# Kernel tuning notes

Measured on AMD Instinct MI355X. Metric: run time of the kernel, lower is better.

The kernel has to match this reference:

```python
import jax, jax.numpy as jnp
import numpy as np

R_ITERS = 3
EPSILON = 1e-7


def squash(s, epsilon=EPSILON, axis=-1):
    # s: (..., dim); v = |s|^2/(1+|s|^2) * s/(|s|+eps)
    s_norm = jnp.linalg.norm(s, axis=axis, keepdims=True)
    sq = jnp.square(s_norm)
    return sq / (1.0 + sq) * (s / (s_norm + epsilon))


def setup_inputs() -> dict:
    key = jax.random.key(0)
    k1, k2 = jax.random.split(key)
    B, P, Dp = 128, 1152, 8     # batch, n_primary_caps, dim_primary_caps
    S, Ds = 32, 16              # n_secondary_caps, dim_secondary_caps
    x = jax.random.normal(k1, (B, P, Dp), dtype=jnp.float32)
    W = jax.random.normal(k2, (S, P, Ds, Dp), dtype=jnp.float32) * 0.05
    return {"x": x, "W": W}


def reference(x, W):
    # u_hat[b,s,p,j] = sum_i W[s,p,j,i] * x[b,p,i]  (replaces tf.map_fn+matmul)
    u_hat = jnp.einsum('spji,bpi->bspj', W, x)  # (B, S, P, Ds)
    B, S, P, Ds = u_hat.shape
    b_logits = jnp.zeros((B, S, P), dtype=u_hat.dtype)
    v = None
    for _ in range(R_ITERS):
        c = jax.nn.softmax(b_logits, axis=-1)                # (B, S, P)
        s_vec = jnp.einsum('bsp,bspj->bsj', c, u_hat)        # (B, S, Ds)
        v = squash(s_vec)                                    # (B, S, Ds)
        agreement = jnp.einsum('bsj,bspj->bsp', v, u_hat)    # (B, S, P)
        b_logits = b_logits + agreement
    return v  # (B, n_secondary_caps, dim_secondary_caps)
```

## Files before the change

kernel.cpp:

```cpp
#include <hip/hip_runtime.h>

#define P_SZ 1152
#define DP 8
#define DS 16
#define NTHR 512
#define NQ 128
#define PT 9
#define NW 8

__global__ __launch_bounds__(NTHR, 4)
void caps_routing5(const float* __restrict__ x, const float* __restrict__ W,
                   float* __restrict__ out) {
    __shared__ float red[2][NW][2][17];

    const int t    = threadIdx.x;
    const int lane = t & 63;
    const int jq   = t & 3;
    const int pq   = t >> 2;
    const int w    = t >> 6;
    const int bid  = blockIdx.x;
    const int s    = bid & 31;
    const int b0   = (bid >> 5) << 1;

    float uh0[PT][4], uh1[PT][4];

    const float* xb0 = x + (size_t)b0 * (P_SZ * DP);
    const float* xb1 = xb0 + P_SZ * DP;

    #pragma unroll
    for (int r = 0; r < PT; ++r) {
        const int p = r * NQ + pq;
        const float* wp = W + (size_t)(s * P_SZ + p) * (DS * DP) + jq * DP;
        const float4 xa0 = *(const float4*)(xb0 + p * DP);
        const float4 xa1 = *(const float4*)(xb0 + p * DP + 4);
        const float4 xc0 = *(const float4*)(xb1 + p * DP);
        const float4 xc1 = *(const float4*)(xb1 + p * DP + 4);
        #pragma unroll
        for (int jj = 0; jj < 4; ++jj) {
            const float4 w0 = *(const float4*)(wp + jj * 32);
            const float4 w1 = *(const float4*)(wp + jj * 32 + 4);
            uh0[r][jj] = w0.x*xa0.x + w0.y*xa0.y + w0.z*xa0.z + w0.w*xa0.w
                       + w1.x*xa1.x + w1.y*xa1.y + w1.z*xa1.z + w1.w*xa1.w;
            uh1[r][jj] = w0.x*xc0.x + w0.y*xc0.y + w0.z*xc0.z + w0.w*xc0.w
                       + w1.x*xc1.x + w1.y*xc1.y + w1.z*xc1.z + w1.w*xc1.w;
        }
    }

    float sv0[4], sv1[4];
    #pragma unroll
    for (int jj = 0; jj < 4; ++jj) {
        float a = 0.f, c = 0.f;
        #pragma unroll
        for (int r = 0; r < PT; ++r) { a += uh0[r][jj]; c += uh1[r][jj]; }
        sv0[jj] = a; sv1[jj] = c;
    }
    #pragma unroll
    for (int off = 4; off < 64; off <<= 1) {
        #pragma unroll
        for (int jj = 0; jj < 4; ++jj) {
            sv0[jj] += __shfl_xor(sv0[jj], off);
            sv1[jj] += __shfl_xor(sv1[jj], off);
        }
    }
    if (lane < 4) {
        #pragma unroll
        for (int jj = 0; jj < 4; ++jj) {
            red[0][w][0][jq + 4*jj] = sv0[jj];
            red[0][w][1][jq + 4*jj] = sv1[jj];
        }
    }
    __syncthreads();
    #pragma unroll
    for (int jj = 0; jj < 4; ++jj) { sv0[jj] = 0.f; sv1[jj] = 0.f; }
    #pragma unroll
    for (int ww = 0; ww < NW; ++ww) {
        #pragma unroll
        for (int jj = 0; jj < 4; ++jj) {
            sv0[jj] += red[0][ww][0][jq + 4*jj];
            sv1[jj] += red[0][ww][1][jq + 4*jj];
        }
    }
    #pragma unroll
    for (int jj = 0; jj < 4; ++jj) { sv0[jj] *= (1.f / P_SZ); sv1[jj] *= (1.f / P_SZ); }

    float sq0 = sv0[0]*sv0[0] + sv0[1]*sv0[1] + sv0[2]*sv0[2] + sv0[3]*sv0[3];
    float sq1 = sv1[0]*sv1[0] + sv1[1]*sv1[1] + sv1[2]*sv1[2] + sv1[3]*sv1[3];
    sq0 += __shfl_xor(sq0, 1); sq0 += __shfl_xor(sq0, 2);
    sq1 += __shfl_xor(sq1, 1); sq1 += __shfl_xor(sq1, 2);
    float f0 = sq0 / (1.f + sq0) / (sqrtf(sq0) + 1e-7f);
    float f1 = sq1 / (1.f + sq1) / (sqrtf(sq1) + 1e-7f);
    float va0[4], va1[4];
    #pragma unroll
    for (int jj = 0; jj < 4; ++jj) { va0[jj] = f0 * sv0[jj]; va1[jj] = f1 * sv1[jj]; }

    #pragma unroll
    for (int it = 1; it < 3; ++it) {
        float es0 = 0.f, es1 = 0.f;
        #pragma unroll
        for (int jj = 0; jj < 4; ++jj) { sv0[jj] = 0.f; sv1[jj] = 0.f; }
        #pragma unroll
        for (int r = 0; r < PT; ++r) {
            float d0 = va0[0]*uh0[r][0] + va0[1]*uh0[r][1]
                     + va0[2]*uh0[r][2] + va0[3]*uh0[r][3];
            float d1 = va1[0]*uh1[r][0] + va1[1]*uh1[r][1]
                     + va1[2]*uh1[r][2] + va1[3]*uh1[r][3];
            d0 += __shfl_xor(d0, 1); d0 += __shfl_xor(d0, 2);
            d1 += __shfl_xor(d1, 1); d1 += __shfl_xor(d1, 2);
            const float e0 = __expf(d0);
            const float e1 = __expf(d1);
            es0 += e0; es1 += e1;
            #pragma unroll
            for (int jj = 0; jj < 4; ++jj) {
                sv0[jj] += e0 * uh0[r][jj];
                sv1[jj] += e1 * uh1[r][jj];
            }
        }
        #pragma unroll
        for (int off = 4; off < 64; off <<= 1) {
            es0 += __shfl_xor(es0, off);
            es1 += __shfl_xor(es1, off);
            #pragma unroll
            for (int jj = 0; jj < 4; ++jj) {
                sv0[jj] += __shfl_xor(sv0[jj], off);
                sv1[jj] += __shfl_xor(sv1[jj], off);
            }
        }
        const int buf = it & 1;
        if (lane < 4) {
            #pragma unroll
            for (int jj = 0; jj < 4; ++jj) {
                red[buf][w][0][jq + 4*jj] = sv0[jj];
                red[buf][w][1][jq + 4*jj] = sv1[jj];
            }
            if (lane == 0) { red[buf][w][0][16] = es0; red[buf][w][1][16] = es1; }
        }
        __syncthreads();
        es0 = 0.f; es1 = 0.f;
        #pragma unroll
        for (int jj = 0; jj < 4; ++jj) { sv0[jj] = 0.f; sv1[jj] = 0.f; }
        #pragma unroll
        for (int ww = 0; ww < NW; ++ww) {
            es0 += red[buf][ww][0][16];
            es1 += red[buf][ww][1][16];
            #pragma unroll
            for (int jj = 0; jj < 4; ++jj) {
                sv0[jj] += red[buf][ww][0][jq + 4*jj];
                sv1[jj] += red[buf][ww][1][jq + 4*jj];
            }
        }
        const float r0 = 1.f / es0, r1 = 1.f / es1;
        #pragma unroll
        for (int jj = 0; jj < 4; ++jj) { sv0[jj] *= r0; sv1[jj] *= r1; }

        sq0 = sv0[0]*sv0[0] + sv0[1]*sv0[1] + sv0[2]*sv0[2] + sv0[3]*sv0[3];
        sq1 = sv1[0]*sv1[0] + sv1[1]*sv1[1] + sv1[2]*sv1[2] + sv1[3]*sv1[3];
        sq0 += __shfl_xor(sq0, 1); sq0 += __shfl_xor(sq0, 2);
        sq1 += __shfl_xor(sq1, 1); sq1 += __shfl_xor(sq1, 2);
        f0 = sq0 / (1.f + sq0) / (sqrtf(sq0) + 1e-7f);
        f1 = sq1 / (1.f + sq1) / (sqrtf(sq1) + 1e-7f);

        if (it == 2) {
            if (t < 4) {
                #pragma unroll
                for (int jj = 0; jj < 4; ++jj)
                    out[(size_t)(b0 * 32 + s) * DS + jq + 4*jj] = f0 * sv0[jj];
            } else if (t < 8) {
                #pragma unroll
                for (int jj = 0; jj < 4; ++jj)
                    out[(size_t)((b0 + 1) * 32 + s) * DS + jq + 4*jj] = f1 * sv1[jj];
            }
        } else {
            #pragma unroll
            for (int jj = 0; jj < 4; ++jj) {
                va0[jj] += f0 * sv0[jj];
                va1[jj] += f1 * sv1[jj];
            }
        }
    }
}

extern "C" void kernel_launch(void* const* d_in, const int* in_sizes, int n_in,
                              void* d_out, int out_size, void* d_ws, size_t ws_size,
                              hipStream_t stream) {
    const float* x = (const float*)d_in[0];
    const float* W = (const float*)d_in[1];
    float* out = (float*)d_out;
    caps_routing5<<<dim3(32 * 64), dim3(NTHR), 0, stream>>>(x, W, out);
}
```

Before: 79.40 us.

## Split each primary capsule's outputs over eight threads with 1024-thread blocks

Doubles the block size to 1024 threads so each capsule row p is handled by 8 threads, each owning 2 of the 16 output dims instead of 4. This halves the per-thread u_hat registers and W loads, giving more waves to hide the latency of the large W stream. In exchange there is an extra shuffle stage per dot product and norm, and twice as many warps write to and read from the shared reduction. The launch-bounds pair (1024, 4) now asks for more resident threads per CU than before, which may tighten the register budget.

```diff
diff --git a/kernel.cpp b/kernel.cpp
--- a/kernel.cpp
+++ b/kernel.cpp
@@ -3,175 +3,173 @@
 #define P_SZ 1152
 #define DP 8
 #define DS 16
-#define NTHR 512
-#define NQ 128
+#define NTHR 1024
 #define PT 9
-#define NW 8
+#define NW 16
 
 __global__ __launch_bounds__(NTHR, 4)
-void caps_routing5(const float* __restrict__ x, const float* __restrict__ W,
+void caps_routing6(const float* __restrict__ x, const float* __restrict__ W,
                    float* __restrict__ out) {
-    __shared__ float red[2][NW][2][17];
+    __shared__ float red[2][NW][2][18];
 
     const int t    = threadIdx.x;
     const int lane = t & 63;
-    const int jq   = t & 3;
-    const int pq   = t >> 2;
+    const int jo   = t & 7;
+    const int po   = t >> 3;
     const int w    = t >> 6;
     const int bid  = blockIdx.x;
     const int s    = bid & 31;
     const int b0   = (bid >> 5) << 1;
 
-    float uh0[PT][4], uh1[PT][4];
+    float uh0[PT][2], uh1[PT][2];
 
     const float* xb0 = x + (size_t)b0 * (P_SZ * DP);
     const float* xb1 = xb0 + P_SZ * DP;
 
     #pragma unroll
     for (int r = 0; r < PT; ++r) {
-        const int p = r * NQ + pq;
-        const float* wp = W + (size_t)(s * P_SZ + p) * (DS * DP) + jq * DP;
+        const int p = (r << 7) + po;
+        const float4* wp = (const float4*)(W + (size_t)(s * P_SZ + p) * (DS * DP) + jo * DP);
+        const float4 w00 = wp[0],  w01 = wp[1];
+        const float4 w10 = wp[16], w11 = wp[17];
         const float4 xa0 = *(const float4*)(xb0 + p * DP);
         const float4 xa1 = *(const float4*)(xb0 + p * DP + 4);
         const float4 xc0 = *(const float4*)(xb1 + p * DP);
         const float4 xc1 = *(const float4*)(xb1 + p * DP + 4);
-        #pragma unroll
-        for (int jj = 0; jj < 4; ++jj) {
-            const float4 w0 = *(const float4*)(wp + jj * 32);
-            const float4 w1 = *(const float4*)(wp + jj * 32 + 4);
-            uh0[r][jj] = w0.x*xa0.x + w0.y*xa0.y + w0.z*xa0.z + w0.w*xa0.w
-                       + w1.x*xa1.x + w1.y*xa1.y + w1.z*xa1.z + w1.w*xa1.w;
-            uh1[r][jj] = w0.x*xc0.x + w0.y*xc0.y + w0.z*xc0.z + w0.w*xc0.w
-                       + w1.x*xc1.x + w1.y*xc1.y + w1.z*xc1.z + w1.w*xc1.w;
-        }
+        uh0[r][0] = w00.x*xa0.x + w00.y*xa0.y + w00.z*xa0.z + w00.w*xa0.w
+                  + w01.x*xa1.x + w01.y*xa1.y + w01.z*xa1.z + w01.w*xa1.w;
+        uh0[r][1] = w10.x*xa0.x + w10.y*xa0.y + w10.z*xa0.z + w10.w*xa0.w
+                  + w11.x*xa1.x + w11.y*xa1.y + w11.z*xa1.z + w11.w*xa1.w;
+        uh1[r][0] = w00.x*xc0.x + w00.y*xc0.y + w00.z*xc0.z + w00.w*xc0.w
+                  + w01.x*xc1.x + w01.y*xc1.y + w01.z*xc1.z + w01.w*xc1.w;
+        uh1[r][1] = w10.x*xc0.x + w10.y*xc0.y + w10.z*xc0.z + w10.w*xc0.w
+                  + w11.x*xc1.x + w11.y*xc1.y + w11.z*xc1.z + w11.w*xc1.w;
     }
 
-    float sv0[4], sv1[4];
+    float sv0[2], sv1[2];
     #pragma unroll
-    for (int jj = 0; jj < 4; ++jj) {
+    for (int jj = 0; jj < 2; ++jj) {
         float a = 0.f, c = 0.f;
         #pragma unroll
         for (int r = 0; r < PT; ++r) { a += uh0[r][jj]; c += uh1[r][jj]; }
         sv0[jj] = a; sv1[jj] = c;
     }
     #pragma unroll
-    for (int off = 4; off < 64; off <<= 1) {
+    for (int off = 8; off < 64; off <<= 1) {
         #pragma unroll
-        for (int jj = 0; jj < 4; ++jj) {
+        for (int jj = 0; jj < 2; ++jj) {
             sv0[jj] += __shfl_xor(sv0[jj], off);
             sv1[jj] += __shfl_xor(sv1[jj], off);
         }
     }
-    if (lane < 4) {
+    if (lane < 8) {
         #pragma unroll
-        for (int jj = 0; jj < 4; ++jj) {
-            red[0][w][0][jq + 4*jj] = sv0[jj];
-            red[0][w][1][jq + 4*jj] = sv1[jj];
+        for (int jj = 0; jj < 2; ++jj) {
+            red[0][w][0][jo + 8*jj] = sv0[jj];
+            red[0][w][1][jo + 8*jj] = sv1[jj];
         }
     }
     __syncthreads();
     #pragma unroll
-    for (int jj = 0; jj < 4; ++jj) { sv0[jj] = 0.f; sv1[jj] = 0.f; }
+    for (int jj = 0; jj < 2; ++jj) { sv0[jj] = 0.f; sv1[jj] = 0.f; }
     #pragma unroll
     for (int ww = 0; ww < NW; ++ww) {
         #pragma unroll
-        for (int jj = 0; jj < 4; ++jj) {
-            sv0[jj] += red[0][ww][0][jq + 4*jj];
-            sv1[jj] += red[0][ww][1][jq + 4*jj];
+        for (int jj = 0; jj < 2; ++jj) {
+            sv0[jj] += red[0][ww][0][jo + 8*jj];
+            sv1[jj] += red[0][ww][1][jo + 8*jj];
         }
     }
     #pragma unroll
-    for (int jj = 0; jj < 4; ++jj) { sv0[jj] *= (1.f / P_SZ); sv1[jj] *= (1.f / P_SZ); }
+    for (int jj = 0; jj < 2; ++jj) { sv0[jj] *= (1.f / P_SZ); sv1[jj] *= (1.f / P_SZ); }
 
-    float sq0 = sv0[0]*sv0[0] + sv0[1]*sv0[1] + sv0[2]*sv0[2] + sv0[3]*sv0[3];
-    float sq1 = sv1[0]*sv1[0] + sv1[1]*sv1[1] + sv1[2]*sv1[2] + sv1[3]*sv1[3];
-    sq0 += __shfl_xor(sq0, 1); sq0 += __shfl_xor(sq0, 2);
-    sq1 += __shfl_xor(sq1, 1); sq1 += __shfl_xor(sq1, 2);
+    float sq0 = sv0[0]*sv0[0] + sv0[1]*sv0[1];
+    float sq1 = sv1[0]*sv1[0] + sv1[1]*sv1[1];
+    sq0 += __shfl_xor(sq0, 1); sq0 += __shfl_xor(sq0, 2); sq0 += __shfl_xor(sq0, 4);
+    sq1 += __shfl_xor(sq1, 1); sq1 += __shfl_xor(sq1, 2); sq1 += __shfl_xor(sq1, 4);
     float f0 = sq0 / (1.f + sq0) / (sqrtf(sq0) + 1e-7f);
     float f1 = sq1 / (1.f + sq1) / (sqrtf(sq1) + 1e-7f);
-    float va0[4], va1[4];
+    float va0[2], va1[2];
     #pragma unroll
-    for (int jj = 0; jj < 4; ++jj) { va0[jj] = f0 * sv0[jj]; va1[jj] = f1 * sv1[jj]; }
+    for (int jj = 0; jj < 2; ++jj) { va0[jj] = f0 * sv0[jj]; va1[jj] = f1 * sv1[jj]; }
 
     #pragma unroll
     for (int it = 1; it < 3; ++it) {
         float es0 = 0.f, es1 = 0.f;
         #pragma unroll
-        for (int jj = 0; jj < 4; ++jj) { sv0[jj] = 0.f; sv1[jj] = 0.f; }
+        for (int jj = 0; jj < 2; ++jj) { sv0[jj] = 0.f; sv1[jj] = 0.f; }
         #pragma unroll
         for (int r = 0; r < PT; ++r) {
-            float d0 = va0[0]*uh0[r][0] + va0[1]*uh0[r][1]
-                     + va0[2]*uh0[r][2] + va0[3]*uh0[r][3];
-            float d1 = va1[0]*uh1[r][0] + va1[1]*uh1[r][1]
-                     + va1[2]*uh1[r][2] + va1[3]*uh1[r][3];
-            d0 += __shfl_xor(d0, 1); d0 += __shfl_xor(d0, 2);
-            d1 += __shfl_xor(d1, 1); d1 += __shfl_xor(d1, 2);
+            float d0 = va0[0]*uh0[r][0] + va0[1]*uh0[r][1];
+            float d1 = va1[0]*uh1[r][0] + va1[1]*uh1[r][1];
+            d0 += __shfl_xor(d0, 1); d0 += __shfl_xor(d0, 2); d0 += __shfl_xor(d0, 4);
+            d1 += __shfl_xor(d1, 1); d1 += __shfl_xor(d1, 2); d1 += __shfl_xor(d1, 4);
             const float e0 = __expf(d0);
             const float e1 = __expf(d1);
             es0 += e0; es1 += e1;
             #pragma unroll
-            for (int jj = 0; jj < 4; ++jj) {
+            for (int jj = 0; jj < 2; ++jj) {
                 sv0[jj] += e0 * uh0[r][jj];
                 sv1[jj] += e1 * uh1[r][jj];
             }
         }
         #pragma unroll
-        for (int off = 4; off < 64; off <<= 1) {
+        for (int off = 8; off < 64; off <<= 1) {
             es0 += __shfl_xor(es0, off);
             es1 += __shfl_xor(es1, off);
             #pragma unroll
-            for (int jj = 0; jj < 4; ++jj) {
+            for (int jj = 0; jj < 2; ++jj) {
                 sv0[jj] += __shfl_xor(sv0[jj], off);
                 sv1[jj] += __shfl_xor(sv1[jj], off);
             }
         }
         const int buf = it & 1;
-        if (lane < 4) {
+        if (lane < 8) {
             #pragma unroll
-            for (int jj = 0; jj < 4; ++jj) {
-                red[buf][w][0][jq + 4*jj] = sv0[jj];
-                red[buf][w][1][jq + 4*jj] = sv1[jj];
+            for (int jj = 0; jj < 2; ++jj) {
+                red[buf][w][0][jo + 8*jj] = sv0[jj];
+                red[buf][w][1][jo + 8*jj] = sv1[jj];
             }
             if (lane == 0) { red[buf][w][0][16] = es0; red[buf][w][1][16] = es1; }
         }
         __syncthreads();
         es0 = 0.f; es1 = 0.f;
         #pragma unroll
-        for (int jj = 0; jj < 4; ++jj) { sv0[jj] = 0.f; sv1[jj] = 0.f; }
+        for (int jj = 0; jj < 2; ++jj) { sv0[jj] = 0.f; sv1[jj] = 0.f; }
         #pragma unroll
         for (int ww = 0; ww < NW; ++ww) {
             es0 += red[buf][ww][0][16];
             es1 += red[buf][ww][1][16];
             #pragma unroll
-            for (int jj = 0; jj < 4; ++jj) {
-                sv0[jj] += red[buf][ww][0][jq + 4*jj];
-                sv1[jj] += red[buf][ww][1][jq + 4*jj];
+            for (int jj = 0; jj < 2; ++jj) {
+                sv0[jj] += red[buf][ww][0][jo + 8*jj];
+                sv1[jj] += red[buf][ww][1][jo + 8*jj];
             }
         }
         const float r0 = 1.f / es0, r1 = 1.f / es1;
         #pragma unroll
-        for (int jj = 0; jj < 4; ++jj) { sv0[jj] *= r0; sv1[jj] *= r1; }
+        for (int jj = 0; jj < 2; ++jj) { sv0[jj] *= r0; sv1[jj] *= r1; }
 
-        sq0 = sv0[0]*sv0[0] + sv0[1]*sv0[1] + sv0[2]*sv0[2] + sv0[3]*sv0[3];
-        sq1 = sv1[0]*sv1[0] + sv1[1]*sv1[1] + sv1[2]*sv1[2] + sv1[3]*sv1[3];
-        sq0 += __shfl_xor(sq0, 1); sq0 += __shfl_xor(sq0, 2);
-        sq1 += __shfl_xor(sq1, 1); sq1 += __shfl_xor(sq1, 2);
+        sq0 = sv0[0]*sv0[0] + sv0[1]*sv0[1];
+        sq1 = sv1[0]*sv1[0] + sv1[1]*sv1[1];
+        sq0 += __shfl_xor(sq0, 1); sq0 += __shfl_xor(sq0, 2); sq0 += __shfl_xor(sq0, 4);
+        sq1 += __shfl_xor(sq1, 1); sq1 += __shfl_xor(sq1, 2); sq1 += __shfl_xor(sq1, 4);
         f0 = sq0 / (1.f + sq0) / (sqrtf(sq0) + 1e-7f);
         f1 = sq1 / (1.f + sq1) / (sqrtf(sq1) + 1e-7f);
 
         if (it == 2) {
-            if (t < 4) {
+            if (t < 8) {
                 #pragma unroll
-                for (int jj = 0; jj < 4; ++jj)
-                    out[(size_t)(b0 * 32 + s) * DS + jq + 4*jj] = f0 * sv0[jj];
-            } else if (t < 8) {
+                for (int jj = 0; jj < 2; ++jj)
+                    out[(size_t)(b0 * 32 + s) * DS + jo + 8*jj] = f0 * sv0[jj];
+            } else if (t < 16) {
                 #pragma unroll
-                for (int jj = 0; jj < 4; ++jj)
-                    out[(size_t)((b0 + 1) * 32 + s) * DS + jq + 4*jj] = f1 * sv1[jj];
+                for (int jj = 0; jj < 2; ++jj)
+                    out[(size_t)((b0 + 1) * 32 + s) * DS + jo + 8*jj] = f1 * sv1[jj];
             }
         } else {
             #pragma unroll
-            for (int jj = 0; jj < 4; ++jj) {
+            for (int jj = 0; jj < 2; ++jj) {
                 va0[jj] += f0 * sv0[jj];
                 va1[jj] += f1 * sv1[jj];
             }
@@ -185,5 +183,5 @@
     const float* x = (const float*)d_in[0];
     const float* W = (const float*)d_in[1];
     float* out = (float*)d_out;
-    caps_routing5<<<dim3(32 * 64), dim3(NTHR), 0, stream>>>(x, W, out);
+    caps_routing6<<<dim3(32 * 64), dim3(NTHR), 0, stream>>>(x, W, out);
 }
```

Measured after the change: 174.6 us. 2.2x slower.
